# Optimization experiments

Measured on AMD Instinct MI355X. Metric: run time of the kernel, lower is better.

The kernel has to match this reference:

```python
import jax, jax.numpy as jnp
import numpy as np
import math
from jax import lax

B, L, C_IN = 32, 1024, 21
D_MODEL, N_HEADS, D_FF = 512, 8, 2048
E_LAYERS, FACTOR, MA_K = 3, 1, 25
N_CLASSES = 10
EPS = 1e-5


def setup_inputs() -> dict:
    key = jax.random.key(0)
    ks = jax.random.split(key, 12)
    s = 0.02
    return {
        "x_enc": jax.random.normal(ks[0], (B, L, C_IN), jnp.float32),
        "x_mark_enc": jnp.ones((B, L), jnp.float32),
        "conv_emb_w": jax.random.normal(ks[1], (D_MODEL, C_IN, 3), jnp.float32) * s,
        "Wq": jax.random.normal(ks[2], (E_LAYERS, D_MODEL, D_MODEL), jnp.float32) * s,
        "bq": jnp.zeros((E_LAYERS, D_MODEL), jnp.float32),
        "Wk": jax.random.normal(ks[3], (E_LAYERS, D_MODEL, D_MODEL), jnp.float32) * s,
        "bk": jnp.zeros((E_LAYERS, D_MODEL), jnp.float32),
        "Wv": jax.random.normal(ks[4], (E_LAYERS, D_MODEL, D_MODEL), jnp.float32) * s,
        "bv": jnp.zeros((E_LAYERS, D_MODEL), jnp.float32),
        "Wo": jax.random.normal(ks[5], (E_LAYERS, D_MODEL, D_MODEL), jnp.float32) * s,
        "bo": jnp.zeros((E_LAYERS, D_MODEL), jnp.float32),
        "Wff1": jax.random.normal(ks[6], (E_LAYERS, D_FF, D_MODEL), jnp.float32) * s,
        "Wff2": jax.random.normal(ks[7], (E_LAYERS, D_MODEL, D_FF), jnp.float32) * s,
        "ln_g": jnp.ones((D_MODEL,), jnp.float32),
        "ln_b": jnp.zeros((D_MODEL,), jnp.float32),
        "Wproj": jax.random.normal(ks[8], (N_CLASSES, D_MODEL * L), jnp.float32) * 0.001,
        "bproj": jnp.zeros((N_CLASSES,), jnp.float32),
    }


def token_embed(x, w):
    # x: [B, L, C] -> Conv1d(C->D, k=3, circular padding, no bias) -> [B, L, D]
    xp = jnp.pad(x.transpose(0, 2, 1), ((0, 0), (0, 0), (1, 1)), mode='wrap')  # [B,C,L+2]
    y = lax.conv_general_dilated(xp, w, (1,), 'VALID', dimension_numbers=('NCH', 'OIH', 'NCH'))
    return y.transpose(0, 2, 1)


def moving_avg(x, k):
    # replicate-pad then avg-pool with stride 1 (kernel k odd -> same length)
    pad = (k - 1) // 2
    xp = jnp.concatenate([jnp.repeat(x[:, :1], pad, 1), x, jnp.repeat(x[:, -1:], pad, 1)], axis=1)
    return lax.reduce_window(xp, 0.0, lax.add, (1, k, 1), (1, 1, 1), 'VALID') / k


def series_decomp(x, k):
    m = moving_avg(x, k)
    return x - m, m


def auto_correlation(q, k, v):
    # q,k,v: [B, L, H, E]; FFT-based period correlation + time-delay aggregation (inference variant)
    B_, L_, H, E = q.shape
    qf = jnp.fft.rfft(q.transpose(0, 2, 3, 1), axis=-1)   # [B,H,E,Lf]
    kf = jnp.fft.rfft(k.transpose(0, 2, 3, 1), axis=-1)
    corr = jnp.fft.irfft(qf * jnp.conj(kf), n=L_, axis=-1)  # [B,H,E,L]
    values = v.transpose(0, 2, 3, 1)                        # [B,H,E,L]
    mean_value = corr.mean(axis=(1, 2))                     # [B,L]
    top_k = int(FACTOR * math.log(L_))
    weights, delay = lax.top_k(mean_value, top_k)           # [B,k]
    tmp_corr = jax.nn.softmax(weights, axis=-1)
    tmp_values = jnp.concatenate([values, values], axis=-1)  # [B,H,E,2L]
    init_index = jnp.arange(L_)
    agg = jnp.zeros_like(values)
    for i in range(top_k):  # small fixed loop (top_k = 6)
        idx = init_index[None, :] + delay[:, i:i + 1]        # [B,L]
        idx_b = jnp.broadcast_to(idx[:, None, None, :], (B_, H, E, L_))
        pat = jnp.take_along_axis(tmp_values, idx_b, axis=-1)
        agg = agg + pat * tmp_corr[:, i][:, None, None, None]
    return agg.transpose(0, 3, 1, 2)  # [B,L,H,E]


def encoder_layer(x, Wq, bq, Wk, bk, Wv, bv, Wo, bo, Wf1, Wf2):
    B_, L_, D = x.shape
    E = D // N_HEADS
    q = (x @ Wq.T + bq).reshape(B_, L_, N_HEADS, E)
    k = (x @ Wk.T + bk).reshape(B_, L_, N_HEADS, E)
    v = (x @ Wv.T + bv).reshape(B_, L_, N_HEADS, E)
    a = auto_correlation(q, k, v).reshape(B_, L_, D)
    a = a @ Wo.T + bo
    x = x + a
    x, _ = series_decomp(x, MA_K)
    y = jax.nn.gelu(jnp.einsum('bld,fd->blf', x, Wf1), approximate=False)
    y = jnp.einsum('blf,df->bld', y, Wf2)
    res, _ = series_decomp(x + y, MA_K)
    return res


def my_layernorm(x, g, b):
    mu = x.mean(-1, keepdims=True)
    var = ((x - mu) ** 2).mean(-1, keepdims=True)
    xh = (x - mu) / jnp.sqrt(var + EPS) * g + b
    return xh - xh.mean(axis=1, keepdims=True)  # special LN: remove seq-wise mean


def reference(x_enc, x_mark_enc, conv_emb_w, Wq, bq, Wk, bk, Wv, bv, Wo, bo, Wff1, Wff2, ln_g, ln_b, Wproj, bproj):
    x = token_embed(x_enc, conv_emb_w)  # DataEmbedding_wo_pos with x_mark=None
    for l in range(E_LAYERS):
        x = encoder_layer(x, Wq[l], bq[l], Wk[l], bk[l], Wv[l], bv[l], Wo[l], bo[l], Wff1[l], Wff2[l])
    x = my_layernorm(x, ln_g, ln_b)
    out = jax.nn.gelu(x, approximate=False)
    out = out * x_mark_enc[:, :, None]
    out = out.reshape(out.shape[0], -1)
    return out @ Wproj.T + bproj
```

## Files before the change

kernel.cpp:

```cpp
#include <hip/hip_runtime.h>
#include <cstdint>


using u16 = unsigned short;
typedef _Float16 f16x8 __attribute__((ext_vector_type(8)));
typedef float f32x4 __attribute__((ext_vector_type(4)));

#define BB 32
#define LL 1024
#define DD 512
#define DFF 2048

__device__ __forceinline__ float bf2f(u16 u) {
  union { uint32_t i; float f; } v; v.i = ((uint32_t)u) << 16; return v.f;
}
__device__ __forceinline__ u16 f2bf(float f) {
  union { float f; uint32_t i; } v; v.f = f;
  uint32_t r = (v.i + 0x7FFFu + ((v.i >> 16) & 1u)) >> 16;
  return (u16)r;
}
__device__ __forceinline__ float ldi(const void* p, long i, int isf) {
  return isf ? ((const float*)p)[i] : bf2f(((const u16*)p)[i]);
}
__device__ __forceinline__ float gelu_f(float x) {
  return 0.5f * x * (1.0f + erff(x * 0.70710678118654752440f));
}
__device__ __forceinline__ void gld16(const void* g, void* l) {
  __builtin_amdgcn_global_load_lds(
      (const __attribute__((address_space(1))) void*)g,
      (__attribute__((address_space(3))) void*)l, 16, 0, 0);
}
__device__ __forceinline__ void swz8(int& bx, int& by) {
  int gx = gridDim.x;
  int nwg = gx * gridDim.y;
  int bid = by * gx + bx;
  int q = nwg >> 3;
  int s = (bid & 7) * q + (bid >> 3);
  bx = s % gx;
  by = s / gx;
}

union H8 { f16x8 v; uint4 u; _Float16 h[8]; };
union H4 { uint2 u; _Float16 h[4]; };

__global__ void detect_k(const uint32_t* __restrict__ mark, int* __restrict__ FLAG) {
  if (threadIdx.x == 0) FLAG[0] = (mark[0] == 0x3F800000u) ? 1 : 0;
}

__global__ __launch_bounds__(256) void wT_k(const void* __restrict__ w,
                                            float* __restrict__ wT,
                                            const int* __restrict__ FLAG) {
  const int isf = *FLAG;
  int idx = blockIdx.x * 256 + threadIdx.x;
  if (idx >= 63 * DD) return;
  int c3t = idx / DD;
  int d = idx - c3t * DD;
  wT[idx] = ldi(w, (long)d * 63 + c3t, isf);
}

__global__ __launch_bounds__(256) void conv_embed_k(
    const void* __restrict__ xe, const float* __restrict__ wT,
    float* __restrict__ X, _Float16* __restrict__ XH, _Float16* __restrict__ XL,
    const int* __restrict__ FLAG) {
  const int isf = *FLAG;
  int b = blockIdx.y;
  int l0 = blockIdx.x * 16;
  __shared__ float xs[18][21];
  int tid = threadIdx.x;
  for (int i = tid; i < 18 * 21; i += 256) {
    int r = i / 21, c = i % 21;
    int row = (l0 - 1 + r + LL) & (LL - 1);
    xs[r][c] = ldi(xe, ((long)b * LL + row) * 21 + c, isf);
  }
  __syncthreads();
  float acc0[16], acc1[16];
#pragma unroll
  for (int ll = 0; ll < 16; ll++) { acc0[ll] = 0.0f; acc1[ll] = 0.0f; }
  for (int c = 0; c < 21; c++) {
    float xreg[18];
#pragma unroll
    for (int r = 0; r < 18; r++) xreg[r] = xs[r][c];
#pragma unroll
    for (int t = 0; t < 3; t++) {
      float w0 = wT[(c * 3 + t) * DD + tid];
      float w1 = wT[(c * 3 + t) * DD + tid + 256];
#pragma unroll
      for (int ll = 0; ll < 16; ll++) {
        acc0[ll] = fmaf(w0, xreg[t + ll], acc0[ll]);
        acc1[ll] = fmaf(w1, xreg[t + ll], acc1[ll]);
      }
    }
  }
#pragma unroll
  for (int ll = 0; ll < 16; ll++) {
    long base = ((long)b * LL + l0 + ll) * DD;
    float v0 = acc0[ll], v1 = acc1[ll];
    X[base + tid] = v0;
    X[base + tid + 256] = v1;
    _Float16 h0 = (_Float16)v0, h1 = (_Float16)v1;
    XH[base + tid] = h0;
    XH[base + tid + 256] = h1;
    XL[base + tid] = (_Float16)((v0 - (float)h0) * 512.0f);
    XL[base + tid + 256] = (_Float16)((v1 - (float)h1) * 512.0f);
  }
}

__global__ __launch_bounds__(256) void tsplit2_k(
    const void* __restrict__ W1, const void* __restrict__ W2, long off,
    _Float16* __restrict__ T1H, _Float16* __restrict__ T1L,
    _Float16* __restrict__ T2H, _Float16* __restrict__ T2L,
    const int* __restrict__ FLAG) {
  const int isf = *FLAG;
  const void* W = blockIdx.z ? W2 : W1;
  _Float16* TH = blockIdx.z ? T2H : T1H;
  _Float16* TL = blockIdx.z ? T2L : T1L;
  __shared__ float t[64][65];
  const int f0 = blockIdx.x * 64, m0 = blockIdx.y * 64;
  const int tid = threadIdx.x;
  const int c = tid & 63, rb = tid >> 6;
#pragma unroll
  for (int r = rb; r < 64; r += 4)
    t[r][c] = ldi(W, off + (long)(f0 + r) * DD + m0 + c, isf);
  __syncthreads();
#pragma unroll
  for (int r = rb; r < 64; r += 4) {
    float v = t[c][r];
    long o = (long)(m0 + r) * DD + f0 + c;
    _Float16 hv = (_Float16)v;
    TH[o] = hv;
    TL[o] = (_Float16)((v - (float)hv) * 512.0f);
  }
}

__global__ __launch_bounds__(256) void split_k(const float* __restrict__ src,
                                               _Float16* __restrict__ dh,
                                               _Float16* __restrict__ dl, int n) {
  long i = ((long)blockIdx.x * 256 + threadIdx.x) * 8;
  if (i >= n) return;
  float4 a = *(const float4*)(src + i);
  float4 b = *(const float4*)(src + i + 4);
  float x[8] = {a.x, a.y, a.z, a.w, b.x, b.y, b.z, b.w};
  H8 h, l;
#pragma unroll
  for (int j = 0; j < 8; j++) {
    _Float16 hv = (_Float16)x[j];
    h.h[j] = hv;
    l.h[j] = (_Float16)((x[j] - (float)hv) * 512.0f);
  }
  *(uint4*)(dh + i) = h.u;
  *(uint4*)(dl + i) = l.u;
}

__global__ __launch_bounds__(256) void wcvt6_k(
    const void* __restrict__ Wv, const void* __restrict__ Wo,
    const void* __restrict__ W1, const void* __restrict__ W2,
    long oW, long oF,
    _Float16* __restrict__ Wvh, _Float16* __restrict__ Woh,
    _Float16* __restrict__ W1h, _Float16* __restrict__ W2h,
    const int* __restrict__ FLAG) {
  const int isf = *FLAG;
  long e = ((long)blockIdx.x * 256 + threadIdx.x) * 8;
  const void* src; long soff; _Float16* dst;
  if (e < 262144) { src = Wv; soff = oW + e; dst = Wvh + e; }
  else if (e < 524288) { src = Wo; soff = oW + (e - 262144); dst = Woh + (e - 262144); }
  else if (e < 1572864) { src = W1; soff = oF + (e - 524288); dst = W1h + (e - 524288); }
  else { src = W2; soff = oF + (e - 1572864); dst = W2h + (e - 1572864); }
  H8 r;
  if (isf) {
    const float* s = (const float*)src + soff;
    float4 a = *(const float4*)s;
    float4 b = *(const float4*)(s + 4);
    r.h[0] = (_Float16)a.x; r.h[1] = (_Float16)a.y;
    r.h[2] = (_Float16)a.z; r.h[3] = (_Float16)a.w;
    r.h[4] = (_Float16)b.x; r.h[5] = (_Float16)b.y;
    r.h[6] = (_Float16)b.z; r.h[7] = (_Float16)b.w;
  } else {
    const u16* s = (const u16*)src + soff;
    uint4 u = *(const uint4*)s;
    r.h[0] = (_Float16)bf2f((u16)(u.x & 0xffff));
    r.h[1] = (_Float16)bf2f((u16)(u.x >> 16));
    r.h[2] = (_Float16)bf2f((u16)(u.y & 0xffff));
    r.h[3] = (_Float16)bf2f((u16)(u.y >> 16));
    r.h[4] = (_Float16)bf2f((u16)(u.z & 0xffff));
    r.h[5] = (_Float16)bf2f((u16)(u.z >> 16));
    r.h[6] = (_Float16)bf2f((u16)(u.w & 0xffff));
    r.h[7] = (_Float16)bf2f((u16)(u.w >> 16));
  }
  *(uint4*)(dst) = r.u;
}

__global__ __launch_bounds__(256) void gemm_z(
    const _Float16* __restrict__ Ah, const _Float16* __restrict__ Al,
    const _Float16* __restrict__ Bh, const _Float16* __restrict__ Bl,
    _Float16* __restrict__ Zh, _Float16* __restrict__ Zl,
    int M, int N, int K) {
  __shared__ __align__(16) _Float16 AsH[2][128 * 32];
  __shared__ __align__(16) _Float16 AsL[2][128 * 32];
  __shared__ __align__(16) _Float16 BsH[2][128 * 32];
  __shared__ __align__(16) _Float16 BsL[2][128 * 32];
  int bx = blockIdx.x, by = blockIdx.y;
  swz8(bx, by);
  const int n0 = bx * 128, m0 = by * 128;
  const int tid = threadIdx.x;
  const int lane = tid & 63, wvi = tid >> 6;
  const int wm = (wvi >> 1) * 64, wn = (wvi & 1) * 64;
  const int l15 = lane & 15, quad = lane >> 4;
  const int ib = wvi * 128 + lane;
  const int r0 = ib >> 2, r1 = r0 + 16;
  const int c0 = ((ib & 3) ^ ((r0 >> 1) & 3)) * 8;
  const int c1 = ((ib & 3) ^ ((r1 >> 1) & 3)) * 8;
  const int lb0 = wvi * 1024, lb1 = wvi * 1024 + 512;
  const long ga0 = (long)(m0 + r0) * K + c0;
  const long ga1 = (long)(m0 + r1) * K + c1;
  const long gb0 = (long)(n0 + r0) * K + c0;
  const long gb1 = (long)(n0 + r1) * K + c1;
  f32x4 aM[4][4], aC[4][4];
#pragma unroll
  for (int i = 0; i < 4; i++)
#pragma unroll
    for (int j = 0; j < 4; j++) {
      aM[i][j] = (f32x4){0.f, 0.f, 0.f, 0.f};
      aC[i][j] = (f32x4){0.f, 0.f, 0.f, 0.f};
    }
  gld16(Ah + ga0, AsH[0] + lb0);
  gld16(Ah + ga1, AsH[0] + lb1);
  gld16(Al + ga0, AsL[0] + lb0);
  gld16(Al + ga1, AsL[0] + lb1);
  gld16(Bh + gb0, BsH[0] + lb0);
  gld16(Bh + gb1, BsH[0] + lb1);
  gld16(Bl + gb0, BsL[0] + lb0);
  gld16(Bl + gb1, BsL[0] + lb1);
  __syncthreads();
  int cur = 0;
  for (int k0 = 0; k0 < K; k0 += 32) {
    const int kn = k0 + 32;
    if (kn < K) {
      gld16(Ah + ga0 + kn, AsH[cur ^ 1] + lb0);
      gld16(Ah + ga1 + kn, AsH[cur ^ 1] + lb1);
      gld16(Al + ga0 + kn, AsL[cur ^ 1] + lb0);
      gld16(Al + ga1 + kn, AsL[cur ^ 1] + lb1);
      gld16(Bh + gb0 + kn, BsH[cur ^ 1] + lb0);
      gld16(Bh + gb1 + kn, BsH[cur ^ 1] + lb1);
      gld16(Bl + gb0 + kn, BsL[cur ^ 1] + lb0);
      gld16(Bl + gb1 + kn, BsL[cur ^ 1] + lb1);
    }
    f16x8 fah[4], fal[4], fbh[4], fbl[4];
#pragma unroll
    for (int mi = 0; mi < 4; mi++) {
      int r = wm + mi * 16 + l15;
      int o = r * 32 + ((quad ^ ((r >> 1) & 3)) * 8);
      fah[mi] = *(const f16x8*)&AsH[cur][o];
      fal[mi] = *(const f16x8*)&AsL[cur][o];
    }
#pragma unroll
    for (int ni = 0; ni < 4; ni++) {
      int r = wn + ni * 16 + l15;
      int o = r * 32 + ((quad ^ ((r >> 1) & 3)) * 8);
      fbh[ni] = *(const f16x8*)&BsH[cur][o];
      fbl[ni] = *(const f16x8*)&BsL[cur][o];
    }
#pragma unroll
    for (int mi = 0; mi < 4; mi++)
#pragma unroll
      for (int ni = 0; ni < 4; ni++) {
        aM[mi][ni] = __builtin_amdgcn_mfma_f32_16x16x32_f16(
            fah[mi], fbh[ni], aM[mi][ni], 0, 0, 0);
        aC[mi][ni] = __builtin_amdgcn_mfma_f32_16x16x32_f16(
            fah[mi], fbl[ni], aC[mi][ni], 0, 0, 0);
        aC[mi][ni] = __builtin_amdgcn_mfma_f32_16x16x32_f16(
            fal[mi], fbh[ni], aC[mi][ni], 0, 0, 0);
      }
    __syncthreads();
    cur ^= 1;
  }
#pragma unroll
  for (int mi = 0; mi < 4; mi++) {
    int rowg = m0 + wm + mi * 16 + quad * 4;
#pragma unroll
    for (int ni = 0; ni < 4; ni++) {
      int colg = n0 + wn + ni * 16 + l15;
#pragma unroll
      for (int rr = 0; rr < 4; rr++) {
        long off = (long)(rowg + rr) * N + colg;
        float z = aM[mi][ni][rr] + aC[mi][ni][rr] * (1.0f / 512.0f);
        _Float16 zh = (_Float16)z;
        Zh[off] = zh;
        Zl[off] = (_Float16)((z - (float)zh) * 512.0f);
      }
    }
  }
}

__global__ __launch_bounds__(256) void qkmv_hl(
    const _Float16* __restrict__ Zh, const _Float16* __restrict__ Zl,
    const _Float16* __restrict__ Xh, const _Float16* __restrict__ Xl,
    float* __restrict__ MV) {
  __shared__ __align__(16) _Float16 AsH[2][128 * 32];
  __shared__ __align__(16) _Float16 AsL[2][128 * 32];
  __shared__ __align__(16) _Float16 BsH[2][128 * 32];
  __shared__ __align__(16) _Float16 BsL[2][128 * 32];
  __shared__ float diag[255];
  const int bz = blockIdx.z;
  const long bb = (long)bz * LL * DD;
  const int n0 = blockIdx.x * 128, m0 = blockIdx.y * 128;
  const int tid = threadIdx.x;
  const int lane = tid & 63, wvi = tid >> 6;
  const int wm = (wvi >> 1) * 64, wn = (wvi & 1) * 64;
  const int l15 = lane & 15, quad = lane >> 4;
  const int ib = wvi * 128 + lane;
  const int r0 = ib >> 2, r1 = r0 + 16;
  const int c0 = ((ib & 3) ^ ((r0 >> 1) & 3)) * 8;
  const int c1 = ((ib & 3) ^ ((r1 >> 1) & 3)) * 8;
  const int lb0 = wvi * 1024, lb1 = wvi * 1024 + 512;
  const long ga0 = bb + (long)(m0 + r0) * DD + c0;
  const long ga1 = bb + (long)(m0 + r1) * DD + c1;
  const long gb0 = bb + (long)(n0 + r0) * DD + c0;
  const long gb1 = bb + (long)(n0 + r1) * DD + c1;
  if (tid < 255) diag[tid] = 0.0f;
  f32x4 aM[4][4], aC[4][4];
#pragma unroll
  for (int i = 0; i < 4; i++)
#pragma unroll
    for (int j = 0; j < 4; j++) {
      aM[i][j] = (f32x4){0.f, 0.f, 0.f, 0.f};
      aC[i][j] = (f32x4){0.f, 0.f, 0.f, 0.f};
    }
  gld16(Zh + ga0, AsH[0] + lb0);
  gld16(Zh + ga1, AsH[0] + lb1);
  gld16(Zl + ga0, AsL[0] + lb0);
  gld16(Zl + ga1, AsL[0] + lb1);
  gld16(Xh + gb0, BsH[0] + lb0);
  gld16(Xh + gb1, BsH[0] + lb1);
  gld16(Xl + gb0, BsL[0] + lb0);
  gld16(Xl + gb1, BsL[0] + lb1);
  __syncthreads();
  int cur = 0;
  for (int k0 = 0; k0 < DD; k0 += 32) {
    const int kn = k0 + 32;
    if (kn < DD) {
      gld16(Zh + ga0 + kn, AsH[cur ^ 1] + lb0);
      gld16(Zh + ga1 + kn, AsH[cur ^ 1] + lb1);
      gld16(Zl + ga0 + kn, AsL[cur ^ 1] + lb0);
      gld16(Zl + ga1 + kn, AsL[cur ^ 1] + lb1);
      gld16(Xh + gb0 + kn, BsH[cur ^ 1] + lb0);
      gld16(Xh + gb1 + kn, BsH[cur ^ 1] + lb1);
      gld16(Xl + gb0 + kn, BsL[cur ^ 1] + lb0);
      gld16(Xl + gb1 + kn, BsL[cur ^ 1] + lb1);
    }
    f16x8 fah[4], fal[4], fbh[4], fbl[4];
#pragma unroll
    for (int mi = 0; mi < 4; mi++) {
      int r = wm + mi * 16 + l15;
      int o = r * 32 + ((quad ^ ((r >> 1) & 3)) * 8);
      fah[mi] = *(const f16x8*)&AsH[cur][o];
      fal[mi] = *(const f16x8*)&AsL[cur][o];
    }
#pragma unroll
    for (int ni = 0; ni < 4; ni++) {
      int r = wn + ni * 16 + l15;
      int o = r * 32 + ((quad ^ ((r >> 1) & 3)) * 8);
      fbh[ni] = *(const f16x8*)&BsH[cur][o];
      fbl[ni] = *(const f16x8*)&BsL[cur][o];
    }
#pragma unroll
    for (int mi = 0; mi < 4; mi++)
#pragma unroll
      for (int ni = 0; ni < 4; ni++) {
        aM[mi][ni] = __builtin_amdgcn_mfma_f32_16x16x32_f16(
            fah[mi], fbh[ni], aM[mi][ni], 0, 0, 0);
        aC[mi][ni] = __builtin_amdgcn_mfma_f32_16x16x32_f16(
            fah[mi], fbl[ni], aC[mi][ni], 0, 0, 0);
        aC[mi][ni] = __builtin_amdgcn_mfma_f32_16x16x32_f16(
            fal[mi], fbh[ni], aC[mi][ni], 0, 0, 0);
      }
    __syncthreads();
    cur ^= 1;
  }
#pragma unroll
  for (int g = -3; g <= 3; g++) {
#pragma unroll
    for (int rr = 0; rr < 4; rr++) {
      float s = 0.0f;
#pragma unroll
      for (int mi = 0; mi < 4; mi++) {
        int ni = mi - g;
        if (ni >= 0 && ni < 4)
          s += aM[mi][ni][rr] + aC[mi][ni][rr] * (1.0f / 512.0f);
      }
      int d = 127 + (wm - wn) + g * 16 + quad * 4 + rr - l15;
      atomicAdd(&diag[d], s);
    }
  }
  __syncthreads();
  if (tid < 255) {
    int tau = (m0 - n0 + tid - 127 + LL) & (LL - 1);
    atomicAdd(&MV[(long)bz * LL + tau], diag[tid] * (1.0f / 512.0f));
  }
}

template <int FLAGS>
__global__ __launch_bounds__(256) void gemm_h(
    const _Float16* __restrict__ A, const _Float16* __restrict__ W,
    const void* __restrict__ biasBase, long bOff,
    const float* __restrict__ R, void* __restrict__ Cout,
    int M, int N, int K, const int* __restrict__ FLAG) {
  constexpr bool HAS_BIAS = (FLAGS & 1) != 0;
  constexpr bool DO_GELU = (FLAGS & 2) != 0;
  constexpr bool DO_RES = (FLAGS & 4) != 0;
  constexpr bool OUT_H = (FLAGS & 8) != 0;
  __shared__ __align__(16) _Float16 As[128 * 64];
  __shared__ __align__(16) _Float16 Bs[128 * 64];
  int bx = blockIdx.x, by = blockIdx.y;
  swz8(bx, by);
  const int n0 = bx * 128, m0 = by * 128;
  const int tid = threadIdx.x;
  const int lane = tid & 63, wvi = tid >> 6;
  const int wm = (wvi >> 1) * 64, wn = (wvi & 1) * 64;
  const int l15 = lane & 15, quad = lane >> 4;
  const _Float16* gA[4];
  const _Float16* gB[4];
  int ldsOff[4];
#pragma unroll
  for (int j = 0; j < 4; j++) {
    int ib = wvi * 256 + j * 64 + lane;
    int row = ib >> 3, p = ib & 7;
    int gc = ((p & 4) | ((p & 3) ^ ((row >> 1) & 3))) * 8;
    gA[j] = A + (long)(m0 + row) * K + gc;
    gB[j] = W + (long)(n0 + row) * K + gc;
    ldsOff[j] = wvi * 2048 + j * 512;
  }
  f32x4 acc[4][4];
#pragma unroll
  for (int i = 0; i < 4; i++)
#pragma unroll
    for (int j = 0; j < 4; j++) acc[i][j] = (f32x4){0.f, 0.f, 0.f, 0.f};
  for (int k0 = 0; k0 < K; k0 += 64) {
    __syncthreads();
#pragma unroll
    for (int j = 0; j < 4; j++) gld16(gA[j] + k0, As + ldsOff[j]);
#pragma unroll
    for (int j = 0; j < 4; j++) gld16(gB[j] + k0, Bs + ldsOff[j]);
    __syncthreads();
#pragma unroll
    for (int ks = 0; ks < 2; ks++) {
      f16x8 af[4], bfr[4];
#pragma unroll
      for (int mi = 0; mi < 4; mi++) {
        int r = wm + mi * 16 + l15;
        af[mi] = *(const f16x8*)&As[r * 64 + (ks * 4 + (quad ^ ((r >> 1) & 3))) * 8];
      }
#pragma unroll
      for (int ni = 0; ni < 4; ni++) {
        int r = wn + ni * 16 + l15;
        bfr[ni] = *(const f16x8*)&Bs[r * 64 + (ks * 4 + (quad ^ ((r >> 1) & 3))) * 8];
      }
#pragma unroll
      for (int mi = 0; mi < 4; mi++)
#pragma unroll
        for (int ni = 0; ni < 4; ni++)
          acc[mi][ni] = __builtin_amdgcn_mfma_f32_16x16x32_f16(
              af[mi], bfr[ni], acc[mi][ni], 0, 0, 0);
    }
  }
  float bcol[4];
  if constexpr (HAS_BIAS) {
    const int isf = *FLAG;
#pragma unroll
    for (int ni = 0; ni < 4; ni++)
      bcol[ni] = ldi(biasBase, bOff + n0 + wn + ni * 16 + l15, isf);
  }
#pragma unroll
  for (int mi = 0; mi < 4; mi++) {
    int rowg = m0 + wm + mi * 16 + quad * 4;
#pragma unroll
    for (int ni = 0; ni < 4; ni++) {
      int colg = n0 + wn + ni * 16 + l15;
#pragma unroll
      for (int rr = 0; rr < 4; rr++) {
        long off = (long)(rowg + rr) * N + colg;
        float v = acc[mi][ni][rr];
        if constexpr (HAS_BIAS) v += bcol[ni];
        if constexpr (DO_RES) v += R[off];
        if constexpr (DO_GELU) v = gelu_f(v);
        if constexpr (OUT_H) ((_Float16*)Cout)[off] = (_Float16)v;
        else ((float*)Cout)[off] = v;
      }
    }
  }
}

__global__ __launch_bounds__(256) void gemm_hf(
    const float* __restrict__ A, const _Float16* __restrict__ W,
    _Float16* __restrict__ Cout, int M, int N, int K) {
  __shared__ __align__(16) float As32[2][128 * 32];
  __shared__ __align__(16) _Float16 Bs[2][128 * 32];
  int bx = blockIdx.x, by = blockIdx.y;
  swz8(bx, by);
  const int n0 = bx * 128, m0 = by * 128;
  const int tid = threadIdx.x;
  const int lane = tid & 63, wvi = tid >> 6;
  const int wm = (wvi >> 1) * 64, wn = (wvi & 1) * 64;
  const int l15 = lane & 15, quad = lane >> 4;
  const float* gAf[4];
#pragma unroll
  for (int j = 0; j < 4; j++) {
    int ib = j * 256 + tid;
    int row = ib >> 3, p = ib & 7;
    int gs = p ^ (row & 7);
    gAf[j] = A + (long)(m0 + row) * K + gs * 4;
  }
  const int ibb = wvi * 128 + lane;
  const int r0 = ibb >> 2, r1 = r0 + 16;
  const int c0 = ((ibb & 3) ^ ((r0 >> 1) & 3)) * 8;
  const int c1 = ((ibb & 3) ^ ((r1 >> 1) & 3)) * 8;
  const int lb0 = wvi * 1024, lb1 = wvi * 1024 + 512;
  const long gb0 = (long)(n0 + r0) * K + c0;
  const long gb1 = (long)(n0 + r1) * K + c1;
  f32x4 acc[4][4];
#pragma unroll
  for (int i = 0; i < 4; i++)
#pragma unroll
    for (int j = 0; j < 4; j++) acc[i][j] = (f32x4){0.f, 0.f, 0.f, 0.f};
#pragma unroll
  for (int j = 0; j < 4; j++)
    gld16(gAf[j], As32[0] + j * 1024 + wvi * 256);
  gld16(W + gb0, Bs[0] + lb0);
  gld16(W + gb1, Bs[0] + lb1);
  __syncthreads();
  int cur = 0;
  for (int k0 = 0; k0 < K; k0 += 32) {
    const int kn = k0 + 32;
    if (kn < K) {
#pragma unroll
      for (int j = 0; j < 4; j++)
        gld16(gAf[j] + kn, As32[cur ^ 1] + j * 1024 + wvi * 256);
      gld16(W + gb0 + kn, Bs[cur ^ 1] + lb0);
      gld16(W + gb1 + kn, Bs[cur ^ 1] + lb1);
    }
    f16x8 af[4], bf[4];
#pragma unroll
    for (int mi = 0; mi < 4; mi++) {
      int r = wm + mi * 16 + l15;
      int p0 = (2 * quad) ^ (r & 7);
      int p1 = (2 * quad + 1) ^ (r & 7);
      f32x4 v0 = *(const f32x4*)&As32[cur][r * 32 + p0 * 4];
      f32x4 v1 = *(const f32x4*)&As32[cur][r * 32 + p1 * 4];
      H8 h;
      h.h[0] = (_Float16)v0[0]; h.h[1] = (_Float16)v0[1];
      h.h[2] = (_Float16)v0[2]; h.h[3] = (_Float16)v0[3];
      h.h[4] = (_Float16)v1[0]; h.h[5] = (_Float16)v1[1];
      h.h[6] = (_Float16)v1[2]; h.h[7] = (_Float16)v1[3];
      af[mi] = h.v;
    }
#pragma unroll
    for (int ni = 0; ni < 4; ni++) {
      int r = wn + ni * 16 + l15;
      int o = r * 32 + ((quad ^ ((r >> 1) & 3)) * 8);
      bf[ni] = *(const f16x8*)&Bs[cur][o];
    }
#pragma unroll
    for (int mi = 0; mi < 4; mi++)
#pragma unroll
      for (int ni = 0; ni < 4; ni++)
        acc[mi][ni] = __builtin_amdgcn_mfma_f32_16x16x32_f16(
            af[mi], bf[ni], acc[mi][ni], 0, 0, 0);
    __syncthreads();
    cur ^= 1;
  }
#pragma unroll
  for (int mi = 0; mi < 4; mi++) {
    int rowg = m0 + wm + mi * 16 + quad * 4;
#pragma unroll
    for (int ni = 0; ni < 4; ni++) {
      int colg = n0 + wn + ni * 16 + l15;
#pragma unroll
      for (int rr = 0; rr < 4; rr++) {
        float v = gelu_f(acc[mi][ni][rr]);
        Cout[(long)(rowg + rr) * N + colg] = (_Float16)v;
      }
    }
  }
}

__global__ __launch_bounds__(256) void topk_k(const float* __restrict__ MV,
                                              float* __restrict__ WGT,
                                              int* __restrict__ DLY) {
  int b = blockIdx.x;
  __shared__ float vals[LL];
  __shared__ float rv[256];
  __shared__ int ri[256];
  __shared__ float selv[6];
  int tid = threadIdx.x;
  for (int i = tid; i < LL; i += 256) vals[i] = MV[(long)b * LL + i];
  __syncthreads();
  for (int it = 0; it < 6; it++) {
    float bv = -1e30f;
    int bi = LL - 1;
    for (int i = tid; i < LL; i += 256) {
      float v = vals[i];
      if (v > bv || (v == bv && i < bi)) { bv = v; bi = i; }
    }
    rv[tid] = bv; ri[tid] = bi;
    __syncthreads();
    for (int st = 128; st > 0; st >>= 1) {
      if (tid < st) {
        float ov = rv[tid + st]; int oi = ri[tid + st];
        if (ov > rv[tid] || (ov == rv[tid] && oi < ri[tid])) {
          rv[tid] = ov; ri[tid] = oi;
        }
      }
      __syncthreads();
    }
    if (tid == 0) {
      selv[it] = rv[0];
      DLY[b * 6 + it] = ri[0];
      vals[ri[0]] = -1e30f;
    }
    __syncthreads();
  }
  if (tid == 0) {
    float mx = selv[0];
    float e[6], s = 0.0f;
    for (int i = 0; i < 6; i++) { e[i] = expf(selv[i] - mx); s += e[i]; }
    for (int i = 0; i < 6; i++) WGT[b * 6 + i] = e[i] / s;
  }
}

__global__ __launch_bounds__(128) void agg_k(const _Float16* __restrict__ V,
                                             const float* __restrict__ WGT,
                                             const int* __restrict__ DLY,
                                             _Float16* __restrict__ O) {
  int l = blockIdx.x, b = blockIdx.y;
  int tid = threadIdx.x;
  float w[6]; int dl[6];
#pragma unroll
  for (int i = 0; i < 6; i++) { w[i] = WGT[b * 6 + i]; dl[i] = DLY[b * 6 + i]; }
  long base = (long)b * LL * DD;
  int d = tid * 4;
  float a0 = 0, a1 = 0, a2 = 0, a3 = 0;
#pragma unroll
  for (int i = 0; i < 6; i++) {
    int row = (l + dl[i]) & (LL - 1);
    H4 t; t.u = *(const uint2*)&V[base + (long)row * DD + d];
    a0 += w[i] * (float)t.h[0];
    a1 += w[i] * (float)t.h[1];
    a2 += w[i] * (float)t.h[2];
    a3 += w[i] * (float)t.h[3];
  }
  H4 r;
  r.h[0] = (_Float16)a0; r.h[1] = (_Float16)a1;
  r.h[2] = (_Float16)a2; r.h[3] = (_Float16)a3;
  *(uint2*)&O[base + (long)l * DD + d] = r.u;
}

__global__ __launch_bounds__(256) void decomp_k(const float* __restrict__ Xin,
                                                float* __restrict__ Out) {
  int d = blockIdx.x * 256 + threadIdx.x;
  int l0 = blockIdx.y * 64;
  int b = blockIdx.z;
  const float* xb = Xin + (long)b * LL * DD + d;
  float* ob = Out + (long)b * LL * DD + d;
  float wsum = 0.0f;
  for (int j = l0 - 12; j <= l0 + 12; j++) {
    int jj = min(max(j, 0), LL - 1);
    wsum += xb[(long)jj * DD];
  }
  for (int l = l0; l < l0 + 64; l++) {
    float xv = xb[(long)l * DD];
    ob[(long)l * DD] = xv - wsum * (1.0f / 25.0f);
    int ja = min(l + 13, LL - 1);
    int jr = max(l - 12, 0);
    wsum += xb[(long)ja * DD] - xb[(long)jr * DD];
  }
}

__global__ __launch_bounds__(256) void ln_k(const float* __restrict__ X,
                                            const void* __restrict__ g,
                                            const void* __restrict__ be,
                                            float* __restrict__ XHo,
                                            const int* __restrict__ FLAG) {
  const int isf = *FLAG;
  int l = blockIdx.x, b = blockIdx.y;
  const float* xr = X + ((long)b * LL + l) * DD;
  int tid = threadIdx.x;
  float x0 = xr[tid], x1 = xr[tid + 256];
  __shared__ float rs[256], rq[256];
  rs[tid] = x0 + x1;
  rq[tid] = x0 * x0 + x1 * x1;
  __syncthreads();
  for (int st = 128; st > 0; st >>= 1) {
    if (tid < st) { rs[tid] += rs[tid + st]; rq[tid] += rq[tid + st]; }
    __syncthreads();
  }
  float mu = rs[0] * (1.0f / 512.0f);
  float var = rq[0] * (1.0f / 512.0f) - mu * mu;
  float rstd = rsqrtf(var + 1e-5f);
  float* o = XHo + ((long)b * LL + l) * DD;
  o[tid] = (x0 - mu) * rstd * ldi(g, tid, isf) + ldi(be, tid, isf);
  o[tid + 256] = (x1 - mu) * rstd * ldi(g, tid + 256, isf) + ldi(be, tid + 256, isf);
}

__global__ __launch_bounds__(256) void colmean_k(const float* __restrict__ XHo,
                                                 float* __restrict__ CMp) {
  int d = blockIdx.x * 256 + threadIdx.x;
  int part = blockIdx.y;
  int b = blockIdx.z;
  const float* p = XHo + (long)b * LL * DD + (long)part * 128 * DD + d;
  float s = 0.0f;
  for (int l = 0; l < 128; l++) s += p[(long)l * DD];
  CMp[((long)part * BB + b) * DD + d] = s;
}

__global__ __launch_bounds__(256) void geluout_k(const float* __restrict__ XHo,
                                                 const float* __restrict__ CMp,
                                                 const void* __restrict__ mark,
                                                 float* __restrict__ OUT,
                                                 const int* __restrict__ FLAG) {
  const int isf = *FLAG;
  int l = blockIdx.x, b = blockIdx.y;
  int tid = threadIdx.x;
  float mk = ldi(mark, (long)b * LL + l, isf);
  long off = ((long)b * LL + l) * DD;
#pragma unroll
  for (int h = 0; h < 2; h++) {
    int d = tid + h * 256;
    float cs = 0.0f;
#pragma unroll
    for (int p = 0; p < 8; p++) cs += CMp[((long)p * BB + b) * DD + d];
    float v = XHo[off + d] - cs * (1.0f / 1024.0f);
    OUT[off + d] = gelu_f(v) * mk;
  }
}

__global__ __launch_bounds__(256) void proj1_k(const float* __restrict__ OUT,
                                               const void* __restrict__ Wp,
                                               float* __restrict__ PB2,
                                               const int* __restrict__ FLAG) {
  const int isf = *FLAG;
  const int blk = blockIdx.x;
  const int tid = threadIdx.x;
  const int wave = tid >> 6, lane = tid & 63;
  const int grp = lane >> 4, ln = lane & 15;
  const long e = (long)blk * 1024 + tid * 4;
  float w[10][4];
  if (isf) {
    const float* wp = (const float*)Wp;
#pragma unroll
    for (int n = 0; n < 10; n++) {
      float4 t = *(const float4*)&wp[(long)n * 524288 + e];
      w[n][0] = t.x; w[n][1] = t.y; w[n][2] = t.z; w[n][3] = t.w;
    }
  } else {
    const u16* wp = (const u16*)Wp;
#pragma unroll
    for (int n = 0; n < 10; n++) {
      uint2 u = *(const uint2*)&wp[(long)n * 524288 + e];
      w[n][0] = bf2f((u16)(u.x & 0xffff));
      w[n][1] = bf2f((u16)(u.x >> 16));
      w[n][2] = bf2f((u16)(u.y & 0xffff));
      w[n][3] = bf2f((u16)(u.y >> 16));
    }
  }
  __shared__ float sm[4][4][BB][16];
  float4 xn = *(const float4*)&OUT[e];
  for (int b = 0; b < BB; b++) {
    float4 x = xn;
    if (b < BB - 1) xn = *(const float4*)&OUT[(long)(b + 1) * 524288 + e];
    float acc[10];
#pragma unroll
    for (int n = 0; n < 10; n++)
      acc[n] = x.x * w[n][0] + x.y * w[n][1] + x.z * w[n][2] + x.w * w[n][3];
#pragma unroll
    for (int s = 1; s <= 8; s <<= 1)
#pragma unroll
      for (int n = 0; n < 10; n++) acc[n] += __shfl_xor(acc[n], s, 64);
    float v = 0.0f;
#pragma unroll
    for (int n = 0; n < 10; n++) v = (ln == n) ? acc[n] : v;
    if (ln < 10) sm[wave][grp][b][ln] = v;
  }
  __syncthreads();
  for (int o = tid; o < BB * 10; o += 256) {
    int b = o / 10, n = o - b * 10;
    float s = 0.0f;
#pragma unroll
    for (int w4 = 0; w4 < 4; w4++)
#pragma unroll
      for (int g = 0; g < 4; g++) s += sm[w4][g][b][n];
    PB2[(long)o * 512 + blk] = s;
  }
}

__global__ __launch_bounds__(64) void proj2_k(const float* __restrict__ PB2,
                                              const void* __restrict__ bp,
                                              void* __restrict__ out,
                                              const int* __restrict__ FLAG) {
  const int isf = *FLAG;
  int n = blockIdx.x, b = blockIdx.y;
  int o = b * 10 + n;
  int tid = threadIdx.x;
  float s = 0.0f;
  for (int j = tid; j < 512; j += 64) s += PB2[(long)o * 512 + j];
#pragma unroll
  for (int st = 32; st > 0; st >>= 1) s += __shfl_xor(s, st, 64);
  if (tid == 0) {
    s += ldi(bp, n, isf);
    if (isf) ((float*)out)[o] = s;
    else ((u16*)out)[o] = f2bf(s);
  }
}

extern "C" void kernel_launch(void* const* d_in, const int* in_sizes, int n_in,
                              void* d_out, int out_size, void* d_ws, size_t ws_size,
                              hipStream_t stream) {
  const void* xe = d_in[0];
  const void* mark = d_in[1];
  const void* cw = d_in[2];
  const void* Wq = d_in[3];
  const void* Wk = d_in[5];
  const void* Wv = d_in[7];
  const void* bv = d_in[8];
  const void* Wo = d_in[9];
  const void* bo = d_in[10];
  const void* Wff1 = d_in[11];
  const void* Wff2 = d_in[12];
  const void* lng = d_in[13];
  const void* lnb = d_in[14];
  const void* Wp = d_in[15];
  const void* bp = d_in[16];

  char* ws = (char*)d_ws;
  float* X      = (float*)(ws + 0L);
  _Float16* XH  = (_Float16*)(ws + 67108864L);
  _Float16* XL  = (_Float16*)(ws + 100663296L);
  _Float16* AGh = (_Float16*)(ws + 100663296L);
  _Float16* ZH  = (_Float16*)(ws + 134217728L);
  _Float16* ZL  = (_Float16*)(ws + 138412032L);
  _Float16* Ph  = (_Float16*)(ws + 134217728L);
  float* CMp    = (float*)(ws + 134217728L);
  float* wT     = (float*)(ws + 142606336L);
  _Float16* KTH = (_Float16*)(ws + 142606336L);
  _Float16* KTL = (_Float16*)(ws + 143130624L);
  _Float16* QTH = (_Float16*)(ws + 143654912L);
  _Float16* QTL = (_Float16*)(ws + 144179200L);
  _Float16* GH  = (_Float16*)(ws + 144703488L);
  _Float16* GL  = (_Float16*)(ws + 145227776L);
  _Float16* Wvh = (_Float16*)(ws + 142606336L);
  _Float16* Woh = (_Float16*)(ws + 143130624L);
  _Float16* W1h = (_Float16*)(ws + 143654912L);
  _Float16* W2h = (_Float16*)(ws + 145752064L);
  float* MV  = (float*)(ws + 147849216L);
  float* WGT = (float*)(ws + 147980288L);
  int*   DLY = (int*)(ws + 147981312L);
  int*  FLAG = (int*)(ws + 148068352L);
  float* S2  = (float*)(ws + 67108864L);
  float* PB2 = (float*)(ws + 67108864L);
  _Float16* Hb = (_Float16*)X;

  const long AD = (long)LL * DD;
  const int M = BB * LL;

  detect_k<<<1, 64, 0, stream>>>((const uint32_t*)mark, FLAG);
  wT_k<<<126, 256, 0, stream>>>(cw, wT, FLAG);
  conv_embed_k<<<dim3(64, 32), 256, 0, stream>>>(xe, wT, X, XH, XL, FLAG);

  for (int l = 0; l < 3; l++) {
    const long oW = (long)l * DD * DD;
    const long oB = (long)l * DD;
    const long oF = (long)l * DFF * DD;

    tsplit2_k<<<dim3(8, 8, 2), 256, 0, stream>>>(Wk, Wq, oW,
                                                 KTH, KTL, QTH, QTL, FLAG);
    gemm_z<<<dim3(4, 4), 256, 0, stream>>>(KTH, KTL, QTH, QTL,
                                           GH, GL, 512, 512, 512);
    hipMemsetAsync(MV, 0, (long)BB * LL * sizeof(float), stream);
    for (int cb = 0; cb < 8; cb++) {
      const long co = (long)cb * 4 * AD;
      gemm_z<<<dim3(4, 32), 256, 0, stream>>>(
          XH + co, XL + co, GH, GL, ZH, ZL, 4096, DD, DD);
      qkmv_hl<<<dim3(8, 8, 4), 256, 0, stream>>>(
          ZH, ZL, XH + co, XL + co, MV + (long)cb * 4 * LL);
    }
    topk_k<<<32, 256, 0, stream>>>(MV, WGT, DLY);

    wcvt6_k<<<1280, 256, 0, stream>>>(Wv, Wo, Wff1, Wff2, oW, oF,
                                      Wvh, Woh, W1h, W2h, FLAG);

    for (int cb = 0; cb < 4; cb++) {
      const _Float16* xh = XH + (long)cb * 8 * AD;
      gemm_h<1 | 8><<<dim3(4, 64), 256, 0, stream>>>(
          xh, Wvh, bv, oB, nullptr, Ph, 8192, DD, DD, FLAG);
      agg_k<<<dim3(1024, 8), 128, 0, stream>>>(
          Ph, WGT + cb * 48, DLY + cb * 48, AGh + (long)cb * 8 * AD);
    }

    gemm_h<1 | 4><<<dim3(4, 256), 256, 0, stream>>>(
        AGh, Woh, bo, oB, X, X, M, DD, DD, FLAG);

    decomp_k<<<dim3(2, 16, 32), 256, 0, stream>>>(X, S2);

    for (int cb = 0; cb < 4; cb++) {
      float* xd = S2 + (long)cb * 8 * AD;
      gemm_hf<<<dim3(16, 64), 256, 0, stream>>>(
          xd, W1h, Hb, 8192, DFF, DD);
      gemm_h<4><<<dim3(4, 64), 256, 0, stream>>>(
          Hb, W2h, nullptr, 0, xd, xd, 8192, DD, DFF, FLAG);
    }

    decomp_k<<<dim3(2, 16, 32), 256, 0, stream>>>(S2, X);
    if (l < 2) split_k<<<8192, 256, 0, stream>>>(X, XH, XL, 16777216);
  }

  ln_k<<<dim3(1024, 32), 256, 0, stream>>>(X, lng, lnb, S2, FLAG);
  colmean_k<<<dim3(2, 8, 32), 256, 0, stream>>>(S2, CMp);
  geluout_k<<<dim3(1024, 32), 256, 0, stream>>>(S2, CMp, mark, X, FLAG);
  proj1_k<<<512, 256, 0, stream>>>(X, Wp, PB2, FLAG);
  proj2_k<<<dim3(10, 32), 64, 0, stream>>>(PB2, bp, d_out, FLAG);
}
```

Baseline: 3.411 ms.

## Double-buffer gemm_h LDS tiles and replace fp32-input FF1 GEMM with fp16 pre-conversion

Restructures gemm_h from a single-buffered 64-wide K tile with two barriers per step to a double-buffered 32-wide K tile that prefetches the next tile while the current one computes, using one barrier per step. The specialised gemm_hf kernel, which loaded fp32 activations and converted them inside the loop, is removed. In its place a separate acvt_k kernel converts each activation chunk to fp16 into the Ph buffer, and the generic gemm_h with GELU and fp16 output runs on it. This overlaps global loads with MFMA work and halves the A-operand bytes in FF1. The cost is an extra kernel launch and an extra write and read of the converted activations per chunk.

After: 3.444 ms. No clear change (+1.0%).

```diff
diff --git a/kernel.cpp b/kernel.cpp
--- a/kernel.cpp
+++ b/kernel.cpp
@@ -149,6 +149,20 @@
   }
   *(uint4*)(dh + i) = h.u;
   *(uint4*)(dl + i) = l.u;
+}
+
+__global__ __launch_bounds__(256) void acvt_k(const float* __restrict__ src,
+                                              _Float16* __restrict__ dst, int n) {
+  long i = ((long)blockIdx.x * 256 + threadIdx.x) * 8;
+  if (i >= n) return;
+  float4 a = *(const float4*)(src + i);
+  float4 b = *(const float4*)(src + i + 4);
+  H8 r;
+  r.h[0] = (_Float16)a.x; r.h[1] = (_Float16)a.y;
+  r.h[2] = (_Float16)a.z; r.h[3] = (_Float16)a.w;
+  r.h[4] = (_Float16)b.x; r.h[5] = (_Float16)b.y;
+  r.h[6] = (_Float16)b.z; r.h[7] = (_Float16)b.w;
+  *(uint4*)(dst + i) = r.u;
 }
 
 __global__ __launch_bounds__(256) void wcvt6_k(
@@ -408,8 +422,8 @@
   constexpr bool DO_GELU = (FLAGS & 2) != 0;
   constexpr bool DO_RES = (FLAGS & 4) != 0;
   constexpr bool OUT_H = (FLAGS & 8) != 0;
-  __shared__ __align__(16) _Float16 As[128 * 64];
-  __shared__ __align__(16) _Float16 Bs[128 * 64];
+  __shared__ __align__(16) _Float16 As[2][128 * 32];
+  __shared__ __align__(16) _Float16 Bs[2][128 * 32];
   int bx = blockIdx.x, by = blockIdx.y;
   swz8(bx, by);
   const int n0 = bx * 128, m0 = by * 128;
@@ -417,50 +431,55 @@
   const int lane = tid & 63, wvi = tid >> 6;
   const int wm = (wvi >> 1) * 64, wn = (wvi & 1) * 64;
   const int l15 = lane & 15, quad = lane >> 4;
-  const _Float16* gA[4];
-  const _Float16* gB[4];
-  int ldsOff[4];
-#pragma unroll
-  for (int j = 0; j < 4; j++) {
-    int ib = wvi * 256 + j * 64 + lane;
-    int row = ib >> 3, p = ib & 7;
-    int gc = ((p & 4) | ((p & 3) ^ ((row >> 1) & 3))) * 8;
-    gA[j] = A + (long)(m0 + row) * K + gc;
-    gB[j] = W + (long)(n0 + row) * K + gc;
-    ldsOff[j] = wvi * 2048 + j * 512;
-  }
+  const int ib = wvi * 128 + lane;
+  const int r0 = ib >> 2, r1 = r0 + 16;
+  const int c0 = ((ib & 3) ^ ((r0 >> 1) & 3)) * 8;
+  const int c1 = ((ib & 3) ^ ((r1 >> 1) & 3)) * 8;
+  const int lb0 = wvi * 1024, lb1 = wvi * 1024 + 512;
+  const long ga0 = (long)(m0 + r0) * K + c0;
+  const long ga1 = (long)(m0 + r1) * K + c1;
+  const long gb0 = (long)(n0 + r0) * K + c0;
+  const long gb1 = (long)(n0 + r1) * K + c1;
   f32x4 acc[4][4];
 #pragma unroll
   for (int i = 0; i < 4; i++)
 #pragma unroll
     for (int j = 0; j < 4; j++) acc[i][j] = (f32x4){0.f, 0.f, 0.f, 0.f};
-  for (int k0 = 0; k0 < K; k0 += 64) {
+  gld16(A + ga0, As[0] + lb0);
+  gld16(A + ga1, As[0] + lb1);
+  gld16(W + gb0, Bs[0] + lb0);
+  gld16(W + gb1, Bs[0] + lb1);
+  __syncthreads();
+  int cur = 0;
+  for (int k0 = 0; k0 < K; k0 += 32) {
+    const int kn = k0 + 32;
+    if (kn < K) {
+      gld16(A + ga0 + kn, As[cur ^ 1] + lb0);
+      gld16(A + ga1 + kn, As[cur ^ 1] + lb1);
+      gld16(W + gb0 + kn, Bs[cur ^ 1] + lb0);
+      gld16(W + gb1 + kn, Bs[cur ^ 1] + lb1);
+    }
+    f16x8 af[4], bfr[4];
+#pragma unroll
+    for (int mi = 0; mi < 4; mi++) {
+      int r = wm + mi * 16 + l15;
+      int o = r * 32 + ((quad ^ ((r >> 1) & 3)) * 8);
+      af[mi] = *(const f16x8*)&As[cur][o];
+    }
+#pragma unroll
+    for (int ni = 0; ni < 4; ni++) {
+      int r = wn + ni * 16 + l15;
+      int o = r * 32 + ((quad ^ ((r >> 1) & 3)) * 8);
+      bfr[ni] = *(const f16x8*)&Bs[cur][o];
+    }
+#pragma unroll
+    for (int mi = 0; mi < 4; mi++)
+#pragma unroll
+      for (int ni = 0; ni < 4; ni++)
+        acc[mi][ni] = __builtin_amdgcn_mfma_f32_16x16x32_f16(
+            af[mi], bfr[ni], acc[mi][ni], 0, 0, 0);
     __syncthreads();
-#pragma unroll
-    for (int j = 0; j < 4; j++) gld16(gA[j] + k0, As + ldsOff[j]);
-#pragma unroll
-    for (int j = 0; j < 4; j++) gld16(gB[j] + k0, Bs + ldsOff[j]);
-    __syncthreads();
-#pragma unroll
-    for (int ks = 0; ks < 2; ks++) {
-      f16x8 af[4], bfr[4];
-#pragma unroll
-      for (int mi = 0; mi < 4; mi++) {
-        int r = wm + mi * 16 + l15;
-        af[mi] = *(const f16x8*)&As[r * 64 + (ks * 4 + (quad ^ ((r >> 1) & 3))) * 8];
-      }
-#pragma unroll
-      for (int ni = 0; ni < 4; ni++) {
-        int r = wn + ni * 16 + l15;
-        bfr[ni] = *(const f16x8*)&Bs[r * 64 + (ks * 4 + (quad ^ ((r >> 1) & 3))) * 8];
-      }
-#pragma unroll
-      for (int mi = 0; mi < 4; mi++)
-#pragma unroll
-        for (int ni = 0; ni < 4; ni++)
-          acc[mi][ni] = __builtin_amdgcn_mfma_f32_16x16x32_f16(
-              af[mi], bfr[ni], acc[mi][ni], 0, 0, 0);
-    }
+    cur ^= 1;
   }
   float bcol[4];
   if constexpr (HAS_BIAS) {
@@ -484,99 +503,6 @@
         if constexpr (DO_GELU) v = gelu_f(v);
         if constexpr (OUT_H) ((_Float16*)Cout)[off] = (_Float16)v;
         else ((float*)Cout)[off] = v;
-      }
-    }
-  }
-}
-
-__global__ __launch_bounds__(256) void gemm_hf(
-    const float* __restrict__ A, const _Float16* __restrict__ W,
-    _Float16* __restrict__ Cout, int M, int N, int K) {
-  __shared__ __align__(16) float As32[2][128 * 32];
-  __shared__ __align__(16) _Float16 Bs[2][128 * 32];
-  int bx = blockIdx.x, by = blockIdx.y;
-  swz8(bx, by);
-  const int n0 = bx * 128, m0 = by * 128;
-  const int tid = threadIdx.x;
-  const int lane = tid & 63, wvi = tid >> 6;
-  const int wm = (wvi >> 1) * 64, wn = (wvi & 1) * 64;
-  const int l15 = lane & 15, quad = lane >> 4;
-  const float* gAf[4];
-#pragma unroll
-  for (int j = 0; j < 4; j++) {
-    int ib = j * 256 + tid;
-    int row = ib >> 3, p = ib & 7;
-    int gs = p ^ (row & 7);
-    gAf[j] = A + (long)(m0 + row) * K + gs * 4;
-  }
-  const int ibb = wvi * 128 + lane;
-  const int r0 = ibb >> 2, r1 = r0 + 16;
-  const int c0 = ((ibb & 3) ^ ((r0 >> 1) & 3)) * 8;
-  const int c1 = ((ibb & 3) ^ ((r1 >> 1) & 3)) * 8;
-  const int lb0 = wvi * 1024, lb1 = wvi * 1024 + 512;
-  const long gb0 = (long)(n0 + r0) * K + c0;
-  const long gb1 = (long)(n0 + r1) * K + c1;
-  f32x4 acc[4][4];
-#pragma unroll
-  for (int i = 0; i < 4; i++)
-#pragma unroll
-    for (int j = 0; j < 4; j++) acc[i][j] = (f32x4){0.f, 0.f, 0.f, 0.f};
-#pragma unroll
-  for (int j = 0; j < 4; j++)
-    gld16(gAf[j], As32[0] + j * 1024 + wvi * 256);
-  gld16(W + gb0, Bs[0] + lb0);
-  gld16(W + gb1, Bs[0] + lb1);
-  __syncthreads();
-  int cur = 0;
-  for (int k0 = 0; k0 < K; k0 += 32) {
-    const int kn = k0 + 32;
-    if (kn < K) {
-#pragma unroll
-      for (int j = 0; j < 4; j++)
-        gld16(gAf[j] + kn, As32[cur ^ 1] + j * 1024 + wvi * 256);
-      gld16(W + gb0 + kn, Bs[cur ^ 1] + lb0);
-      gld16(W + gb1 + kn, Bs[cur ^ 1] + lb1);
-    }
-    f16x8 af[4], bf[4];
-#pragma unroll
-    for (int mi = 0; mi < 4; mi++) {
-      int r = wm + mi * 16 + l15;
-      int p0 = (2 * quad) ^ (r & 7);
-      int p1 = (2 * quad + 1) ^ (r & 7);
-      f32x4 v0 = *(const f32x4*)&As32[cur][r * 32 + p0 * 4];
-      f32x4 v1 = *(const f32x4*)&As32[cur][r * 32 + p1 * 4];
-      H8 h;
-      h.h[0] = (_Float16)v0[0]; h.h[1] = (_Float16)v0[1];
-      h.h[2] = (_Float16)v0[2]; h.h[3] = (_Float16)v0[3];
-      h.h[4] = (_Float16)v1[0]; h.h[5] = (_Float16)v1[1];
-      h.h[6] = (_Float16)v1[2]; h.h[7] = (_Float16)v1[3];
-      af[mi] = h.v;
-    }
-#pragma unroll
-    for (int ni = 0; ni < 4; ni++) {
-      int r = wn + ni * 16 + l15;
-      int o = r * 32 + ((quad ^ ((r >> 1) & 3)) * 8);
-      bf[ni] = *(const f16x8*)&Bs[cur][o];
-    }
-#pragma unroll
-    for (int mi = 0; mi < 4; mi++)
-#pragma unroll
-      for (int ni = 0; ni < 4; ni++)
-        acc[mi][ni] = __builtin_amdgcn_mfma_f32_16x16x32_f16(
-            af[mi], bf[ni], acc[mi][ni], 0, 0, 0);
-    __syncthreads();
-    cur ^= 1;
-  }
-#pragma unroll
-  for (int mi = 0; mi < 4; mi++) {
-    int rowg = m0 + wm + mi * 16 + quad * 4;
-#pragma unroll
-    for (int ni = 0; ni < 4; ni++) {
-      int colg = n0 + wn + ni * 16 + l15;
-#pragma unroll
-      for (int rr = 0; rr < 4; rr++) {
-        float v = gelu_f(acc[mi][ni][rr]);
-        Cout[(long)(rowg + rr) * N + colg] = (_Float16)v;
       }
     }
   }
@@ -901,8 +827,9 @@
 
     for (int cb = 0; cb < 4; cb++) {
       float* xd = S2 + (long)cb * 8 * AD;
-      gemm_hf<<<dim3(16, 64), 256, 0, stream>>>(
-          xd, W1h, Hb, 8192, DFF, DD);
+      acvt_k<<<2048, 256, 0, stream>>>(xd, Ph, 4194304);
+      gemm_h<2 | 8><<<dim3(16, 64), 256, 0, stream>>>(
+          Ph, W1h, nullptr, 0, nullptr, Hb, 8192, DFF, DD, FLAG);
       gemm_h<4><<<dim3(4, 64), 256, 0, stream>>>(
           Hb, W2h, nullptr, 0, xd, xd, 8192, DD, DFF, FLAG);
     }
```
